# Kernel optimization log

Measured on AMD Instinct MI355X. Metric: run time of the kernel, lower is better.

The kernel has to match this reference:

```python
import jax, jax.numpy as jnp
import numpy as np

NOISE_SCALE = 0.1  # init_kwargs['noise_scale']


def setup_inputs() -> dict:
    key = jax.random.key(0)
    k_x, k_b, k_e, k_p = jax.random.split(key, 4)
    B, F, NB = 65536, 256, 16
    x = jax.random.normal(k_x, (B, F), dtype=jnp.float32)
    # per-feature sorted bin edges spanning roughly the data range [-3, 3]
    bins = jnp.sort(jax.random.uniform(k_b, (F, NB + 1), dtype=jnp.float32,
                                       minval=-3.0, maxval=3.0), axis=1)
    eps = jax.random.normal(k_e, (B, F), dtype=jnp.float32)  # stands in for torch.randn per bin
    noise_params = jnp.zeros((F * NB,), dtype=jnp.float32)   # nn.Parameter init = zeros
    return {"x": x, "bins": bins, "eps": eps, "noise_params": noise_params}


def reference(x, bins, eps, noise_params):
    B, F = x.shape
    params = noise_params.reshape(F, -1)           # [F, n_bins]
    n_bins = params.shape[1]
    # bucketize: for each feature i, idx such that bins[i, idx] <= x < bins[i, idx+1]
    # searchsorted(side='right') returns count of edges <= v; subtract 1 -> bin index
    idx = jax.vmap(lambda b, v: jnp.searchsorted(b, v, side='right'),
                   in_axes=(0, 1), out_axes=1)(bins, x) - 1   # [B, F]
    valid = (idx >= 0) & (idx < n_bins)            # values outside edges get no noise
    jc = jnp.clip(idx, 0, n_bins - 1)
    # gather per-(sample, feature) noise scale: params[feature, bin]
    scale = jax.nn.sigmoid(params[jnp.arange(F)[None, :], jc])  # [B, F]
    noise = jnp.where(valid, eps * scale * NOISE_SCALE, 0.0)
    return x + noise
```

## Files before the change

### kernel.cpp

```cpp
#include <hip/hip_runtime.h>


#define NFEAT 256
#define NBINS 16
#define NEDGE 17
#define NOISE_SCALE 0.1f

__global__ __launch_bounds__(256, 8) void noise_learn_kernel(
    const float* __restrict__ x,
    const float* __restrict__ bins,
    const float* __restrict__ eps,
    const float* __restrict__ params,
    float* __restrict__ out,
    int total2)
{
    __shared__ float s_mem[NEDGE * NFEAT];

    const int t = threadIdx.x;

    #pragma unroll
    for (int i = t; i < NEDGE * NFEAT; i += 256)
        s_mem[i] = bins[i];
    __syncthreads();

    const int gid = blockIdx.x * 256 + t;
    const int f0 = (gid & 127) * 2;
    const int f1 = f0 + 1;

    float e0[NEDGE], e1[NEDGE];
    #pragma unroll
    for (int e = 0; e < NEDGE; ++e) {
        e0[e] = s_mem[f0 * NEDGE + e];
        e1[e] = s_mem[f1 * NEDGE + e];
    }
    __syncthreads();

    #pragma unroll
    for (int k = 0; k < NBINS; ++k) {
        float p = params[t * NBINS + k];
        s_mem[k * NFEAT + t] = 1.0f / (1.0f + expf(-p));
    }
    __syncthreads();

    const int stride = gridDim.x * 256;
    for (int g = gid; g < total2; g += stride) {
        const float2 xv = reinterpret_cast<const float2*>(x)[g];
        const float2 ev = reinterpret_cast<const float2*>(eps)[g];

        int c0 = 0, c1 = 0;
        #pragma unroll
        for (int e = 0; e < NEDGE; ++e) {
            c0 += (e0[e] <= xv.x) ? 1 : 0;
            c1 += (e1[e] <= xv.y) ? 1 : 0;
        }

        float2 ov;
        {
            const int idx = c0 - 1;
            const int jc = idx < 0 ? 0 : (idx > NBINS - 1 ? NBINS - 1 : idx);
            const float sc = s_mem[jc * NFEAT + f0];
            ov.x = xv.x + (((unsigned)idx < (unsigned)NBINS) ? ev.x * sc * NOISE_SCALE : 0.0f);
        }
        {
            const int idx = c1 - 1;
            const int jc = idx < 0 ? 0 : (idx > NBINS - 1 ? NBINS - 1 : idx);
            const float sc = s_mem[jc * NFEAT + f1];
            ov.y = xv.y + (((unsigned)idx < (unsigned)NBINS) ? ev.y * sc * NOISE_SCALE : 0.0f);
        }

        reinterpret_cast<float2*>(out)[g] = ov;
    }
}

extern "C" void kernel_launch(void* const* d_in, const int* in_sizes, int n_in,
                              void* d_out, int out_size, void* d_ws, size_t ws_size,
                              hipStream_t stream) {
    const float* x      = (const float*)d_in[0];
    const float* bins   = (const float*)d_in[1];
    const float* eps    = (const float*)d_in[2];
    const float* params = (const float*)d_in[3];
    float* out = (float*)d_out;

    const int total2 = out_size / 2;
    dim3 block(256);
    dim3 grid(2048);
    noise_learn_kernel<<<grid, block, 0, stream>>>(x, bins, eps, params, out, total2);
}
```

Baseline: 43.36 us.

## Map one feature per thread with scalar loads and direct edge register loads

Each thread now handles one scalar element per iteration, with its feature fixed to the thread index. Because stride and block size are multiples of 256, each thread keeps a single feature's 17 bin edges in registers, loaded straight from global memory without staging through shared memory. Shared memory now holds only the sigmoid table, filled in one pass with fast exp, so one barrier is removed. The trade is float2 vector loads swapped for scalar loads, twice as many loop iterations, and the occupancy hint dropped from launch bounds.

```diff
diff --git a/kernel.cpp b/kernel.cpp
--- a/kernel.cpp
+++ b/kernel.cpp
@@ -6,69 +6,50 @@
 #define NEDGE 17
 #define NOISE_SCALE 0.1f
 
-__global__ __launch_bounds__(256, 8) void noise_learn_kernel(
+__global__ __launch_bounds__(256) void noise_learn_kernel(
     const float* __restrict__ x,
     const float* __restrict__ bins,
     const float* __restrict__ eps,
     const float* __restrict__ params,
     float* __restrict__ out,
-    int total2)
+    int total)
 {
-    __shared__ float s_mem[NEDGE * NFEAT];
+    __shared__ float s_scale[NBINS * NFEAT];
 
     const int t = threadIdx.x;
 
     #pragma unroll
-    for (int i = t; i < NEDGE * NFEAT; i += 256)
-        s_mem[i] = bins[i];
+    for (int i = t; i < NFEAT * NBINS; i += 256) {
+        const float p = params[i];
+        const int f = i >> 4;
+        const int k = i & (NBINS - 1);
+        s_scale[k * NFEAT + f] = 1.0f / (1.0f + __expf(-p));
+    }
+
+    float e[NEDGE];
+    #pragma unroll
+    for (int i = 0; i < NEDGE; ++i)
+        e[i] = bins[t * NEDGE + i];
+
     __syncthreads();
 
     const int gid = blockIdx.x * 256 + t;
-    const int f0 = (gid & 127) * 2;
-    const int f1 = f0 + 1;
+    const int stride = gridDim.x * 256;
 
-    float e0[NEDGE], e1[NEDGE];
-    #pragma unroll
-    for (int e = 0; e < NEDGE; ++e) {
-        e0[e] = s_mem[f0 * NEDGE + e];
-        e1[e] = s_mem[f1 * NEDGE + e];
-    }
-    __syncthreads();
+    for (int g = gid; g < total; g += stride) {
+        const float xv = x[g];
+        const float ev = eps[g];
 
-    #pragma unroll
-    for (int k = 0; k < NBINS; ++k) {
-        float p = params[t * NBINS + k];
-        s_mem[k * NFEAT + t] = 1.0f / (1.0f + expf(-p));
-    }
-    __syncthreads();
+        int c = 0;
+        #pragma unroll
+        for (int i = 0; i < NEDGE; ++i)
+            c += (e[i] <= xv) ? 1 : 0;
 
-    const int stride = gridDim.x * 256;
-    for (int g = gid; g < total2; g += stride) {
-        const float2 xv = reinterpret_cast<const float2*>(x)[g];
-        const float2 ev = reinterpret_cast<const float2*>(eps)[g];
+        const int idx = c - 1;
+        const int jc = idx < 0 ? 0 : (idx > NBINS - 1 ? NBINS - 1 : idx);
+        const float sc = s_scale[jc * NFEAT + t];
 
-        int c0 = 0, c1 = 0;
-        #pragma unroll
-        for (int e = 0; e < NEDGE; ++e) {
-            c0 += (e0[e] <= xv.x) ? 1 : 0;
-            c1 += (e1[e] <= xv.y) ? 1 : 0;
-        }
-
-        float2 ov;
-        {
-            const int idx = c0 - 1;
-            const int jc = idx < 0 ? 0 : (idx > NBINS - 1 ? NBINS - 1 : idx);
-            const float sc = s_mem[jc * NFEAT + f0];
-            ov.x = xv.x + (((unsigned)idx < (unsigned)NBINS) ? ev.x * sc * NOISE_SCALE : 0.0f);
-        }
-        {
-            const int idx = c1 - 1;
-            const int jc = idx < 0 ? 0 : (idx > NBINS - 1 ? NBINS - 1 : idx);
-            const float sc = s_mem[jc * NFEAT + f1];
-            ov.y = xv.y + (((unsigned)idx < (unsigned)NBINS) ? ev.y * sc * NOISE_SCALE : 0.0f);
-        }
-
-        reinterpret_cast<float2*>(out)[g] = ov;
+        out[g] = xv + (((unsigned)idx < (unsigned)NBINS) ? ev * sc * NOISE_SCALE : 0.0f);
     }
 }
 
@@ -81,8 +62,7 @@
     const float* params = (const float*)d_in[3];
     float* out = (float*)d_out;
 
-    const int total2 = out_size / 2;
     dim3 block(256);
     dim3 grid(2048);
-    noise_learn_kernel<<<grid, block, 0, stream>>>(x, bins, eps, params, out, total2);
+    noise_learn_kernel<<<grid, block, 0, stream>>>(x, bins, eps, params, out, out_size);
 }
```

New measurement: 54.62 us. +26.0%, slower.
